# Performance work log

Hardware: AMD Instinct MI355X
Metric: run time of the kernel (lower is better)

## Reference

```python
import jax, jax.numpy as jnp
import numpy as np

DIM_IN = 1024
DIM_OUT = 1024
N_HOST = 4096
N_GUEST = 8192


def setup_inputs() -> dict:
    key = jax.random.key(0)
    k1, k2, k3, k4, k5 = jax.random.split(key, 5)
    # kaiming_uniform_ default: bound = sqrt(6 / fan_in) with a=sqrt(5) -> gain=sqrt(2/(1+5)); here approximate with uniform init
    bound = float(np.sqrt(6.0 / DIM_IN) / np.sqrt(3.0))
    features_host = jax.random.normal(k1, (N_HOST, DIM_IN), dtype=jnp.float32)
    features_guests = jax.random.normal(k2, (N_GUEST, DIM_IN), dtype=jnp.float32)
    Q = jax.random.uniform(k3, (DIM_IN, DIM_OUT), dtype=jnp.float32, minval=-bound, maxval=bound)
    K = jax.random.uniform(k4, (DIM_IN, DIM_OUT), dtype=jnp.float32, minval=-bound, maxval=bound)
    V = jax.random.uniform(k5, (DIM_IN, DIM_OUT), dtype=jnp.float32, minval=-bound, maxval=bound)
    return {"features_host": features_host, "features_guests": features_guests, "Q": Q, "K": K, "V": V}


def reference(features_host, features_guests, Q, K, V):
    # query: [N, d_out], key/value: [M, d_out]
    query = features_host @ Q
    key = features_guests @ K
    value = features_guests @ V
    scale = 1.0 / jnp.sqrt(jnp.asarray(DIM_OUT, dtype=query.dtype))
    att = jnp.einsum("nd,md->nm", query, key) * scale  # [N, M]
    attention = jax.nn.softmax(att, axis=1)
    # dropout(p=0.2) is identity in eval mode (deterministic reference)
    return attention @ value  # [N, d_out]
```

## Files before the change

### kernel.cpp

```cpp
#include <hip/hip_runtime.h>
#include <stdint.h>

typedef float f32x4 __attribute__((ext_vector_type(4)));
typedef short bf16x8 __attribute__((ext_vector_type(8)));
typedef unsigned short u16;
typedef u16 u16x4 __attribute__((ext_vector_type(4)));

__device__ __forceinline__ u16 f2bf(float f) {
    union { float f; uint32_t u; } v; v.f = f;
    uint32_t r = v.u + 0x7FFFu + ((v.u >> 16) & 1u);
    return (u16)(r >> 16);
}
__device__ __forceinline__ float bf2f(u16 b) {
    union { uint32_t u; float f; } v; v.u = ((uint32_t)b) << 16;
    return v.f;
}

__device__ __forceinline__ void gload16(u16* lds, const u16* g) {
    __builtin_amdgcn_global_load_lds(
        (const __attribute__((address_space(1))) void*)(uintptr_t)g,
        (__attribute__((address_space(3))) void*)(uint32_t)(uintptr_t)lds,
        16, 0, 0);
}

__device__ __forceinline__ int xcd_map(int bid, int nwg) {
    return (bid & 7) * (nwg >> 3) + (bid >> 3);
}

#define BK 32

__global__ __launch_bounds__(256)
void proj_gemm(const u16* __restrict__ host_bf, const u16* __restrict__ guests_bf,
               const u16* __restrict__ Qt, const u16* __restrict__ Kt,
               const u16* __restrict__ Vt,
               u16* __restrict__ query_bf, u16* __restrict__ key_bf,
               u16* __restrict__ value_t)
{
    __shared__ u16 a_s[128 * BK];
    __shared__ u16 b_s[128 * BK];
    const int id = xcd_map(blockIdx.x, 1280);

    const u16 *A, *B; u16* Crm = nullptr; int bm, bn; int group;
    if (id < 256)      { group = 0; A = host_bf;   B = Qt; Crm = query_bf; bm = (id >> 3) * 128;         bn = (id & 7) * 128; }
    else if (id < 768) { group = 1; A = guests_bf; B = Kt; Crm = key_bf;   bm = ((id - 256) >> 3) * 128; bn = ((id - 256) & 7) * 128; }
    else               { group = 2; A = guests_bf; B = Vt; Crm = nullptr;  bm = ((id - 768) >> 3) * 128; bn = ((id - 768) & 7) * 128; }

    const int tid  = threadIdx.x;
    const int lane = tid & 63;
    const int wid  = tid >> 6;
    const int lr   = lane & 15;
    const int kg   = lane >> 4;
    const int wm   = (wid >> 1) * 64;
    const int wn   = (wid & 1) * 64;
    const int srow = tid >> 2;
    const int scol = (tid & 3) * 8;

    const u16* Ar0 = A + (size_t)(bm + srow) * 1024 + scol;
    const u16* Ar1 = A + (size_t)(bm + 64 + srow) * 1024 + scol;
    const u16* Br0 = B + (size_t)(bn + srow) * 1024 + scol;
    const u16* Br1 = B + (size_t)(bn + 64 + srow) * 1024 + scol;
    u16* a_d0 = a_s + wid * 512;
    u16* a_d1 = a_s + 2048 + wid * 512;
    u16* b_d0 = b_s + wid * 512;
    u16* b_d1 = b_s + 2048 + wid * 512;

    f32x4 acc[4][4];
#pragma unroll
    for (int i = 0; i < 4; ++i)
#pragma unroll
        for (int j = 0; j < 4; ++j)
            acc[i][j] = (f32x4){0.f, 0.f, 0.f, 0.f};

    for (int k0 = 0; k0 < 1024; k0 += BK) {
        __syncthreads();
        gload16(a_d0, Ar0 + k0);
        gload16(a_d1, Ar1 + k0);
        gload16(b_d0, Br0 + k0);
        gload16(b_d1, Br1 + k0);
        __syncthreads();

        bf16x8 af[4], bfr[4];
#pragma unroll
        for (int i = 0; i < 4; ++i)
            af[i] = *(const bf16x8*)&a_s[(wm + i * 16 + lr) * BK + kg * 8];
#pragma unroll
        for (int j = 0; j < 4; ++j)
            bfr[j] = *(const bf16x8*)&b_s[(wn + j * 16 + lr) * BK + kg * 8];
#pragma unroll
        for (int i = 0; i < 4; ++i)
#pragma unroll
            for (int j = 0; j < 4; ++j)
                acc[i][j] = __builtin_amdgcn_mfma_f32_16x16x32_bf16(af[i], bfr[j], acc[i][j], 0, 0, 0);
    }

    const int r0 = kg * 4;
    if (group == 2) {
#pragma unroll
        for (int i = 0; i < 4; ++i) {
#pragma unroll
            for (int j = 0; j < 4; ++j) {
                const int col = bn + wn + j * 16 + lr;
                const int row = bm + wm + i * 16 + r0;
                u16x4 w;
#pragma unroll
                for (int r = 0; r < 4; ++r) w[r] = f2bf(acc[i][j][r]);
                *(u16x4*)&value_t[(size_t)col * 8192 + row] = w;
            }
        }
    } else {
        const float scale = (group == 0) ? 0.03125f : 1.0f;
#pragma unroll
        for (int i = 0; i < 4; ++i) {
#pragma unroll
            for (int j = 0; j < 4; ++j) {
                const int col = bn + wn + j * 16 + lr;
#pragma unroll
                for (int r = 0; r < 4; ++r) {
                    const int row = bm + wm + i * 16 + r0 + r;
                    Crm[(size_t)row * 1024 + col] = f2bf(acc[i][j][r] * scale);
                }
            }
        }
    }
}

__global__ __launch_bounds__(256)
void qkt_gemm(const u16* __restrict__ A, const u16* __restrict__ Bt,
              u16* __restrict__ Cb)
{
    __shared__ u16 a_s[128 * BK];
    __shared__ u16 b_s[128 * BK];
    const int lin = blockIdx.x + (blockIdx.y << 6);
    const int swz = xcd_map(lin, 2048);
    const int bm = (swz >> 6) * 128;
    const int bn = (swz & 63) * 128;

    const int tid  = threadIdx.x;
    const int lane = tid & 63;
    const int wid  = tid >> 6;
    const int lr   = lane & 15;
    const int kg   = lane >> 4;
    const int wm   = (wid >> 1) * 64;
    const int wn   = (wid & 1) * 64;
    const int srow = tid >> 2;
    const int scol = (tid & 3) * 8;

    const u16* Ar0 = A  + (size_t)(bm + srow) * 1024 + scol;
    const u16* Ar1 = A  + (size_t)(bm + 64 + srow) * 1024 + scol;
    const u16* Br0 = Bt + (size_t)(bn + srow) * 1024 + scol;
    const u16* Br1 = Bt + (size_t)(bn + 64 + srow) * 1024 + scol;
    u16* a_d0 = a_s + wid * 512;
    u16* a_d1 = a_s + 2048 + wid * 512;
    u16* b_d0 = b_s + wid * 512;
    u16* b_d1 = b_s + 2048 + wid * 512;

    f32x4 acc[4][4];
#pragma unroll
    for (int i = 0; i < 4; ++i)
#pragma unroll
        for (int j = 0; j < 4; ++j)
            acc[i][j] = (f32x4){0.f, 0.f, 0.f, 0.f};

    for (int k0 = 0; k0 < 1024; k0 += BK) {
        __syncthreads();
        gload16(a_d0, Ar0 + k0);
        gload16(a_d1, Ar1 + k0);
        gload16(b_d0, Br0 + k0);
        gload16(b_d1, Br1 + k0);
        __syncthreads();

        bf16x8 af[4], bfr[4];
#pragma unroll
        for (int i = 0; i < 4; ++i)
            af[i] = *(const bf16x8*)&a_s[(wm + i * 16 + lr) * BK + kg * 8];
#pragma unroll
        for (int j = 0; j < 4; ++j)
            bfr[j] = *(const bf16x8*)&b_s[(wn + j * 16 + lr) * BK + kg * 8];
#pragma unroll
        for (int i = 0; i < 4; ++i)
#pragma unroll
            for (int j = 0; j < 4; ++j)
                acc[i][j] = __builtin_amdgcn_mfma_f32_16x16x32_bf16(af[i], bfr[j], acc[i][j], 0, 0, 0);
    }

    const int r0 = kg * 4;
#pragma unroll
    for (int i = 0; i < 4; ++i) {
#pragma unroll
        for (int j = 0; j < 4; ++j) {
            const int col = bn + wn + j * 16 + lr;
#pragma unroll
            for (int r = 0; r < 4; ++r) {
                const int row = bm + wm + i * 16 + r0 + r;
                Cb[(size_t)row * 8192 + col] = f2bf(acc[i][j][r]);
            }
        }
    }
}

__global__ __launch_bounds__(256)
void pv_gemm(const u16* __restrict__ A, const u16* __restrict__ Bt,
             float* __restrict__ C0, float* __restrict__ C1, float* __restrict__ C2)
{
    __shared__ u16 a_s[128 * BK];
    __shared__ u16 b_s[128 * BK];
    const int swz = xcd_map(blockIdx.x, 768);
    const int z   = swz >> 8;
    const int rem = swz & 255;
    const int bm  = (rem >> 3) * 128;
    const int bn  = (rem & 7) * 128;

    const int tid  = threadIdx.x;
    const int lane = tid & 63;
    const int wid  = tid >> 6;
    const int lr   = lane & 15;
    const int kg   = lane >> 4;
    const int wm   = (wid >> 1) * 64;
    const int wn   = (wid & 1) * 64;
    const int srow = tid >> 2;
    const int scol = (tid & 3) * 8;

    const int kBeg = z * 2752;
    const int kEnd = (z == 2) ? 8192 : kBeg + 2752;
    float* Cv = (z == 0) ? C0 : (z == 1) ? C1 : C2;

    const u16* Ar0 = A  + (size_t)(bm + srow) * 8192 + scol;
    const u16* Ar1 = A  + (size_t)(bm + 64 + srow) * 8192 + scol;
    const u16* Br0 = Bt + (size_t)(bn + srow) * 8192 + scol;
    const u16* Br1 = Bt + (size_t)(bn + 64 + srow) * 8192 + scol;
    u16* a_d0 = a_s + wid * 512;
    u16* a_d1 = a_s + 2048 + wid * 512;
    u16* b_d0 = b_s + wid * 512;
    u16* b_d1 = b_s + 2048 + wid * 512;

    f32x4 acc[4][4];
#pragma unroll
    for (int i = 0; i < 4; ++i)
#pragma unroll
        for (int j = 0; j < 4; ++j)
            acc[i][j] = (f32x4){0.f, 0.f, 0.f, 0.f};

    for (int k0 = kBeg; k0 < kEnd; k0 += BK) {
        __syncthreads();
        gload16(a_d0, Ar0 + k0);
        gload16(a_d1, Ar1 + k0);
        gload16(b_d0, Br0 + k0);
        gload16(b_d1, Br1 + k0);
        __syncthreads();

        bf16x8 af[4], bfr[4];
#pragma unroll
        for (int i = 0; i < 4; ++i)
            af[i] = *(const bf16x8*)&a_s[(wm + i * 16 + lr) * BK + kg * 8];
#pragma unroll
        for (int j = 0; j < 4; ++j)
            bfr[j] = *(const bf16x8*)&b_s[(wn + j * 16 + lr) * BK + kg * 8];
#pragma unroll
        for (int i = 0; i < 4; ++i)
#pragma unroll
            for (int j = 0; j < 4; ++j)
                acc[i][j] = __builtin_amdgcn_mfma_f32_16x16x32_bf16(af[i], bfr[j], acc[i][j], 0, 0, 0);
    }

    const int r0 = kg * 4;
#pragma unroll
    for (int i = 0; i < 4; ++i) {
#pragma unroll
        for (int j = 0; j < 4; ++j) {
            const int col = bn + wn + j * 16 + lr;
#pragma unroll
            for (int r = 0; r < 4; ++r) {
                const int row = bm + wm + i * 16 + r0 + r;
                Cv[(size_t)row * 1024 + col] = acc[i][j][r];
            }
        }
    }
}

__global__ __launch_bounds__(256)
void wtrans(const float* __restrict__ Qw, const float* __restrict__ Kw,
            const float* __restrict__ Vw, u16* __restrict__ Qt,
            u16* __restrict__ Kt, u16* __restrict__ Vt)
{
    __shared__ u16 tile[64][65];
    const float* in = (blockIdx.z == 0) ? Qw : (blockIdx.z == 1) ? Kw : Vw;
    u16* out        = (blockIdx.z == 0) ? Qt : (blockIdx.z == 1) ? Kt : Vt;
    const int r0 = blockIdx.y * 64;
    const int c0 = blockIdx.x * 64;
    const int tr = threadIdx.x >> 2;
    const int tq = threadIdx.x & 3;

    const float* p = in + (size_t)(r0 + tr) * 1024 + c0 + tq * 16;
#pragma unroll
    for (int i = 0; i < 16; i += 4) {
        float4 v = *(const float4*)(p + i);
        tile[tq * 16 + i + 0][tr] = f2bf(v.x);
        tile[tq * 16 + i + 1][tr] = f2bf(v.y);
        tile[tq * 16 + i + 2][tr] = f2bf(v.z);
        tile[tq * 16 + i + 3][tr] = f2bf(v.w);
    }
    __syncthreads();

    u16 tmp[16];
#pragma unroll
    for (int i = 0; i < 16; ++i) tmp[i] = tile[tr][tq * 16 + i];
    bf16x8 w0, w1;
#pragma unroll
    for (int j = 0; j < 8; ++j) { w0[j] = (short)tmp[j]; w1[j] = (short)tmp[8 + j]; }
    u16* o = out + (size_t)(c0 + tr) * 1024 + r0 + tq * 16;
    *(bf16x8*)o       = w0;
    *(bf16x8*)(o + 8) = w1;
}

__global__ __launch_bounds__(256)
void cvt_inputs(const float* __restrict__ host, const float* __restrict__ guests,
                u16* __restrict__ host_bf, u16* __restrict__ guests_bf)
{
    int b = blockIdx.x;
    const float* in; u16* out;
    if (b < 2048) { in = host; out = host_bf; }
    else          { in = guests; out = guests_bf; b -= 2048; }
    const size_t i = ((size_t)b * 256 + threadIdx.x) * 8;
    float4 v0 = *(const float4*)(in + i);
    float4 v1 = *(const float4*)(in + i + 4);
    bf16x8 w;
    w[0] = (short)f2bf(v0.x); w[1] = (short)f2bf(v0.y);
    w[2] = (short)f2bf(v0.z); w[3] = (short)f2bf(v0.w);
    w[4] = (short)f2bf(v1.x); w[5] = (short)f2bf(v1.y);
    w[6] = (short)f2bf(v1.z); w[7] = (short)f2bf(v1.w);
    *(bf16x8*)(out + i) = w;
}

__global__ __launch_bounds__(256)
void add2_f32(float* __restrict__ out, const float* __restrict__ p1,
              const float* __restrict__ p2)
{
    const size_t i = ((size_t)blockIdx.x * 256 + threadIdx.x) * 4;
    float4 a = *(const float4*)(out + i);
    float4 b = *(const float4*)(p1 + i);
    float4 c = *(const float4*)(p2 + i);
    a.x += b.x + c.x; a.y += b.y + c.y; a.z += b.z + c.z; a.w += b.w + c.w;
    *(float4*)(out + i) = a;
}

__global__ __launch_bounds__(256)
void softmax_inplace(u16* __restrict__ att)
{
    const int tid = threadIdx.x;
    u16* p = att + (size_t)blockIdx.x * 8192;

    float x[32];
#pragma unroll
    for (int c = 0; c < 4; ++c) {
        bf16x8 v = *(const bf16x8*)(p + c * 2048 + tid * 8);
#pragma unroll
        for (int j = 0; j < 8; ++j) x[c * 8 + j] = bf2f((u16)v[j]);
    }

    float mx = -1e30f;
#pragma unroll
    for (int i = 0; i < 32; ++i) mx = fmaxf(mx, x[i]);
#pragma unroll
    for (int o = 32; o >= 1; o >>= 1) mx = fmaxf(mx, __shfl_xor(mx, o));

    __shared__ float red[8];
    const int wid = tid >> 6, lane = tid & 63;
    if (lane == 0) red[wid] = mx;
    __syncthreads();
    mx = fmaxf(fmaxf(red[0], red[1]), fmaxf(red[2], red[3]));

    float s = 0.f;
#pragma unroll
    for (int i = 0; i < 32; ++i) { x[i] = __expf(x[i] - mx); s += x[i]; }
#pragma unroll
    for (int o = 32; o >= 1; o >>= 1) s += __shfl_xor(s, o);
    if (lane == 0) red[4 + wid] = s;
    __syncthreads();
    s = red[4] + red[5] + red[6] + red[7];
    const float inv = 1.0f / s;

#pragma unroll
    for (int c = 0; c < 4; ++c) {
        bf16x8 w;
#pragma unroll
        for (int j = 0; j < 8; ++j) w[j] = (short)f2bf(x[c * 8 + j] * inv);
        *(bf16x8*)(p + c * 2048 + tid * 8) = w;
    }
}

extern "C" void kernel_launch(void* const* d_in, const int* in_sizes, int n_in,
                              void* d_out, int out_size, void* d_ws, size_t ws_size,
                              hipStream_t stream)
{
    const float* host   = (const float*)d_in[0];
    const float* guests = (const float*)d_in[1];
    const float* Qw     = (const float*)d_in[2];
    const float* Kw     = (const float*)d_in[3];
    const float* Vw     = (const float*)d_in[4];
    float* out = (float*)d_out;

    char* ws = (char*)d_ws;
    u16* att       = (u16*)(ws);
    u16* host_bf   = (u16*)(ws);
    u16* guests_bf = (u16*)(ws + ( 8ull << 20));
    u16* Qt        = (u16*)(ws + (24ull << 20));
    u16* Kt        = (u16*)(ws + (26ull << 20));
    u16* Vt        = (u16*)(ws + (28ull << 20));
    u16* query_bf  = (u16*)(ws + (64ull << 20));
    u16* key_bf    = (u16*)(ws + (72ull << 20));
    u16* value_t   = (u16*)(ws + (88ull << 20));
    float* part1   = (float*)(ws + (64ull << 20));
    float* part2   = (float*)(ws + (104ull << 20));

    dim3 blk(256);

    cvt_inputs<<<dim3(6144), blk, 0, stream>>>(host, guests, host_bf, guests_bf);
    wtrans<<<dim3(16, 16, 3), blk, 0, stream>>>(Qw, Kw, Vw, Qt, Kt, Vt);

    proj_gemm<<<dim3(1280), blk, 0, stream>>>(host_bf, guests_bf, Qt, Kt, Vt,
                                              query_bf, key_bf, value_t);

    qkt_gemm<<<dim3(64, 32), blk, 0, stream>>>(query_bf, key_bf, att);

    softmax_inplace<<<dim3(4096), blk, 0, stream>>>(att);

    pv_gemm<<<dim3(768), blk, 0, stream>>>(att, value_t, out, part1, part2);
    add2_f32<<<dim3(4096), blk, 0, stream>>>(out, part1, part2);
}
```

Baseline: 384.9 us.

## Replace QK^T and PV GEMMs with 256x256 double-buffered 8-wave pipelined kernel

Introduces a shared 256x256-tile GEMM core with 512 threads, BK=64, double-buffered LDS (128KB), an XOR-swizzled LDS layout, and interleaved global-to-LDS prefetch and MFMA phases using setprio and fine-grained barriers. The old 128x128 single-buffered kernels are replaced for both the score GEMM and the split-K PV GEMM. The aim is more data reuse per tile, hidden load latency and fewer LDS bank conflicts. In exchange, register pressure and LDS use per block go up. The PV grid shrinks to 192 blocks, which may underfill the CUs.

```diff
diff --git a/kernel.cpp b/kernel.cpp
--- a/kernel.cpp
+++ b/kernel.cpp
@@ -28,6 +28,205 @@
 }
 
 #define BK 32
+
+__device__ __forceinline__ void gemm256_core(
+    const u16* __restrict__ A, const u16* __restrict__ Bt,
+    int lda, int ldb, int bm, int bn, int kBeg, int nt,
+    u16* lds, f32x4 (&acc)[8][4])
+{
+    const int tid  = threadIdx.x;
+    const int lane = tid & 63;
+    const int wid  = tid >> 6;
+    const int lr   = lane & 15;
+    const int kg   = lane >> 4;
+    const int wr   = wid >> 2;
+    const int wc   = wid & 3;
+
+    const int sr = tid >> 3;
+    const int sc = ((tid & 7) ^ (sr & 7)) * 8;
+    const u16* As = A  + (size_t)(bm + sr) * lda + kBeg + sc;
+    const u16* Bs = Bt + (size_t)(bn + sr) * ldb + kBeg + sc;
+    const int ldsW = wid * 512;
+
+    int arow[8], brow[4], kc[2];
+#pragma unroll
+    for (int m = 0; m < 8; ++m) arow[m] = wr * 8192 + (m * 16 + lr) * 64;
+#pragma unroll
+    for (int n = 0; n < 4; ++n)
+        brow[n] = 16384 + (wc >> 1) * 8192 + ((wc & 1) * 64 + n * 16 + lr) * 64;
+#pragma unroll
+    for (int ks = 0; ks < 2; ++ks) kc[ks] = (ks * 32 + kg * 8) ^ ((lr & 7) * 8);
+
+#define STG_A(q, h, t) do { \
+        const u16* _s = As + (size_t)((h) * 128) * lda + (t) * 64; \
+        gload16(lds + (q) * 32768 + (h) * 8192 + ldsW, _s); \
+        gload16(lds + (q) * 32768 + (h) * 8192 + 4096 + ldsW, _s + (size_t)64 * lda); \
+    } while (0)
+#define STG_B(q, h, t) do { \
+        const u16* _s = Bs + (size_t)((h) * 128) * ldb + (t) * 64; \
+        gload16(lds + (q) * 32768 + 16384 + (h) * 8192 + ldsW, _s); \
+        gload16(lds + (q) * 32768 + 16384 + (h) * 8192 + 4096 + ldsW, _s + (size_t)64 * ldb); \
+    } while (0)
+
+    STG_A(0, 0, 0); STG_A(0, 1, 0); STG_B(0, 0, 0); STG_B(0, 1, 0);
+    STG_B(1, 0, 1); STG_B(1, 1, 1);
+    asm volatile("s_waitcnt vmcnt(4)" ::: "memory");
+    __builtin_amdgcn_s_barrier();
+
+    bf16x8 fa[4][2], fb[4][2];
+    for (int t = 0; t < nt; ++t) {
+        const int p  = t & 1;
+        const int pb = p * 32768;
+
+#pragma unroll
+        for (int m = 0; m < 4; ++m)
+#pragma unroll
+            for (int ks = 0; ks < 2; ++ks)
+                fa[m][ks] = *(const bf16x8*)&lds[pb + arow[m] + kc[ks]];
+#pragma unroll
+        for (int n = 0; n < 2; ++n)
+#pragma unroll
+            for (int ks = 0; ks < 2; ++ks)
+                fb[n][ks] = *(const bf16x8*)&lds[pb + brow[n] + kc[ks]];
+        if (t + 1 < nt) STG_A(p ^ 1, 0, t + 1);
+        __builtin_amdgcn_s_barrier();
+        asm volatile("s_waitcnt lgkmcnt(0)" ::: "memory");
+        __builtin_amdgcn_sched_barrier(0);
+        __builtin_amdgcn_s_setprio(1);
+#pragma unroll
+        for (int ks = 0; ks < 2; ++ks)
+#pragma unroll
+            for (int m = 0; m < 4; ++m)
+#pragma unroll
+                for (int n = 0; n < 2; ++n)
+                    acc[m][n] = __builtin_amdgcn_mfma_f32_16x16x32_bf16(fa[m][ks], fb[n][ks], acc[m][n], 0, 0, 0);
+        __builtin_amdgcn_s_setprio(0);
+        __builtin_amdgcn_s_barrier();
+
+#pragma unroll
+        for (int n = 2; n < 4; ++n)
+#pragma unroll
+            for (int ks = 0; ks < 2; ++ks)
+                fb[n][ks] = *(const bf16x8*)&lds[pb + brow[n] + kc[ks]];
+        if (t + 1 < nt) STG_A(p ^ 1, 1, t + 1);
+        __builtin_amdgcn_s_barrier();
+        asm volatile("s_waitcnt lgkmcnt(0)" ::: "memory");
+        __builtin_amdgcn_sched_barrier(0);
+        __builtin_amdgcn_s_setprio(1);
+#pragma unroll
+        for (int ks = 0; ks < 2; ++ks)
+#pragma unroll
+            for (int m = 0; m < 4; ++m)
+#pragma unroll
+                for (int n = 2; n < 4; ++n)
+                    acc[m][n] = __builtin_amdgcn_mfma_f32_16x16x32_bf16(fa[m][ks], fb[n][ks], acc[m][n], 0, 0, 0);
+        __builtin_amdgcn_s_setprio(0);
+        __builtin_amdgcn_s_barrier();
+
+#pragma unroll
+        for (int m = 0; m < 4; ++m)
+#pragma unroll
+            for (int ks = 0; ks < 2; ++ks)
+                fa[m][ks] = *(const bf16x8*)&lds[pb + arow[4 + m] + kc[ks]];
+        if (t + 2 < nt) STG_B(p, 0, t + 2);
+        __builtin_amdgcn_s_barrier();
+        asm volatile("s_waitcnt lgkmcnt(0)" ::: "memory");
+        __builtin_amdgcn_sched_barrier(0);
+        __builtin_amdgcn_s_setprio(1);
+#pragma unroll
+        for (int ks = 0; ks < 2; ++ks)
+#pragma unroll
+            for (int m = 0; m < 4; ++m)
+#pragma unroll
+                for (int n = 0; n < 2; ++n)
+                    acc[4 + m][n] = __builtin_amdgcn_mfma_f32_16x16x32_bf16(fa[m][ks], fb[n][ks], acc[4 + m][n], 0, 0, 0);
+        __builtin_amdgcn_s_setprio(0);
+        __builtin_amdgcn_s_barrier();
+
+        if (t + 2 < nt) STG_B(p, 1, t + 2);
+        __builtin_amdgcn_s_barrier();
+        __builtin_amdgcn_s_setprio(1);
+#pragma unroll
+        for (int ks = 0; ks < 2; ++ks)
+#pragma unroll
+            for (int m = 0; m < 4; ++m)
+#pragma unroll
+                for (int n = 2; n < 4; ++n)
+                    acc[4 + m][n] = __builtin_amdgcn_mfma_f32_16x16x32_bf16(fa[m][ks], fb[n][ks], acc[4 + m][n], 0, 0, 0);
+        __builtin_amdgcn_s_setprio(0);
+        if (t + 2 < nt)      asm volatile("s_waitcnt vmcnt(4)" ::: "memory");
+        else if (t + 1 < nt) asm volatile("s_waitcnt vmcnt(0)" ::: "memory");
+        __builtin_amdgcn_s_barrier();
+    }
+#undef STG_A
+#undef STG_B
+}
+
+__global__ __launch_bounds__(512, 2)
+void qkt256(const u16* __restrict__ A, const u16* __restrict__ Bt,
+            u16* __restrict__ C)
+{
+    __shared__ u16 lds[65536];
+    const int swz = xcd_map(blockIdx.x, 512);
+    const int bm = (swz >> 5) * 256;
+    const int bn = (swz & 31) * 256;
+    f32x4 acc[8][4];
+#pragma unroll
+    for (int m = 0; m < 8; ++m)
+#pragma unroll
+        for (int n = 0; n < 4; ++n) acc[m][n] = (f32x4){0.f, 0.f, 0.f, 0.f};
+    gemm256_core(A, Bt, 1024, 1024, bm, bn, 0, 16, lds, acc);
+
+    const int lane = threadIdx.x & 63, wid = threadIdx.x >> 6;
+    const int lr = lane & 15, kg = lane >> 4, wr = wid >> 2, wc = wid & 3;
+#pragma unroll
+    for (int m = 0; m < 8; ++m)
+#pragma unroll
+        for (int n = 0; n < 4; ++n) {
+            const int col = bn + wc * 64 + n * 16 + lr;
+#pragma unroll
+            for (int r = 0; r < 4; ++r) {
+                const int row = bm + wr * 128 + m * 16 + kg * 4 + r;
+                C[(size_t)row * 8192 + col] = f2bf(acc[m][n][r]);
+            }
+        }
+}
+
+__global__ __launch_bounds__(512, 2)
+void pv256(const u16* __restrict__ A, const u16* __restrict__ Bt,
+           float* __restrict__ C0, float* __restrict__ C1, float* __restrict__ C2)
+{
+    __shared__ u16 lds[65536];
+    const int swz = xcd_map(blockIdx.x, 192);
+    const int z   = swz >> 6;
+    const int rem = swz & 63;
+    const int bm  = (rem >> 2) * 256;
+    const int bn  = (rem & 3) * 256;
+    const int kBeg = z * 2752;
+    const int nt   = (z == 2) ? 42 : 43;
+    float* Cv = (z == 0) ? C0 : (z == 1) ? C1 : C2;
+
+    f32x4 acc[8][4];
+#pragma unroll
+    for (int m = 0; m < 8; ++m)
+#pragma unroll
+        for (int n = 0; n < 4; ++n) acc[m][n] = (f32x4){0.f, 0.f, 0.f, 0.f};
+    gemm256_core(A, Bt, 8192, 8192, bm, bn, kBeg, nt, lds, acc);
+
+    const int lane = threadIdx.x & 63, wid = threadIdx.x >> 6;
+    const int lr = lane & 15, kg = lane >> 4, wr = wid >> 2, wc = wid & 3;
+#pragma unroll
+    for (int m = 0; m < 8; ++m)
+#pragma unroll
+        for (int n = 0; n < 4; ++n) {
+            const int col = bn + wc * 64 + n * 16 + lr;
+#pragma unroll
+            for (int r = 0; r < 4; ++r) {
+                const int row = bm + wr * 128 + m * 16 + kg * 4 + r;
+                Cv[(size_t)row * 1024 + col] = acc[m][n][r];
+            }
+        }
+}
 
 __global__ __launch_bounds__(256)
 void proj_gemm(const u16* __restrict__ host_bf, const u16* __restrict__ guests_bf,
@@ -119,159 +318,6 @@
                     const int row = bm + wm + i * 16 + r0 + r;
                     Crm[(size_t)row * 1024 + col] = f2bf(acc[i][j][r] * scale);
                 }
-            }
-        }
-    }
-}
-
-__global__ __launch_bounds__(256)
-void qkt_gemm(const u16* __restrict__ A, const u16* __restrict__ Bt,
-              u16* __restrict__ Cb)
-{
-    __shared__ u16 a_s[128 * BK];
-    __shared__ u16 b_s[128 * BK];
-    const int lin = blockIdx.x + (blockIdx.y << 6);
-    const int swz = xcd_map(lin, 2048);
-    const int bm = (swz >> 6) * 128;
-    const int bn = (swz & 63) * 128;
-
-    const int tid  = threadIdx.x;
-    const int lane = tid & 63;
-    const int wid  = tid >> 6;
-    const int lr   = lane & 15;
-    const int kg   = lane >> 4;
-    const int wm   = (wid >> 1) * 64;
-    const int wn   = (wid & 1) * 64;
-    const int srow = tid >> 2;
-    const int scol = (tid & 3) * 8;
-
-    const u16* Ar0 = A  + (size_t)(bm + srow) * 1024 + scol;
-    const u16* Ar1 = A  + (size_t)(bm + 64 + srow) * 1024 + scol;
-    const u16* Br0 = Bt + (size_t)(bn + srow) * 1024 + scol;
-    const u16* Br1 = Bt + (size_t)(bn + 64 + srow) * 1024 + scol;
-    u16* a_d0 = a_s + wid * 512;
-    u16* a_d1 = a_s + 2048 + wid * 512;
-    u16* b_d0 = b_s + wid * 512;
-    u16* b_d1 = b_s + 2048 + wid * 512;
-
-    f32x4 acc[4][4];
-#pragma unroll
-    for (int i = 0; i < 4; ++i)
-#pragma unroll
-        for (int j = 0; j < 4; ++j)
-            acc[i][j] = (f32x4){0.f, 0.f, 0.f, 0.f};
-
-    for (int k0 = 0; k0 < 1024; k0 += BK) {
-        __syncthreads();
-        gload16(a_d0, Ar0 + k0);
-        gload16(a_d1, Ar1 + k0);
-        gload16(b_d0, Br0 + k0);
-        gload16(b_d1, Br1 + k0);
-        __syncthreads();
-
-        bf16x8 af[4], bfr[4];
-#pragma unroll
-        for (int i = 0; i < 4; ++i)
-            af[i] = *(const bf16x8*)&a_s[(wm + i * 16 + lr) * BK + kg * 8];
-#pragma unroll
-        for (int j = 0; j < 4; ++j)
-            bfr[j] = *(const bf16x8*)&b_s[(wn + j * 16 + lr) * BK + kg * 8];
-#pragma unroll
-        for (int i = 0; i < 4; ++i)
-#pragma unroll
-            for (int j = 0; j < 4; ++j)
-                acc[i][j] = __builtin_amdgcn_mfma_f32_16x16x32_bf16(af[i], bfr[j], acc[i][j], 0, 0, 0);
-    }
-
-    const int r0 = kg * 4;
-#pragma unroll
-    for (int i = 0; i < 4; ++i) {
-#pragma unroll
-        for (int j = 0; j < 4; ++j) {
-            const int col = bn + wn + j * 16 + lr;
-#pragma unroll
-            for (int r = 0; r < 4; ++r) {
-                const int row = bm + wm + i * 16 + r0 + r;
-                Cb[(size_t)row * 8192 + col] = f2bf(acc[i][j][r]);
-            }
-        }
-    }
-}
-
-__global__ __launch_bounds__(256)
-void pv_gemm(const u16* __restrict__ A, const u16* __restrict__ Bt,
-             float* __restrict__ C0, float* __restrict__ C1, float* __restrict__ C2)
-{
-    __shared__ u16 a_s[128 * BK];
-    __shared__ u16 b_s[128 * BK];
-    const int swz = xcd_map(blockIdx.x, 768);
-    const int z   = swz >> 8;
-    const int rem = swz & 255;
-    const int bm  = (rem >> 3) * 128;
-    const int bn  = (rem & 7) * 128;
-
-    const int tid  = threadIdx.x;
-    const int lane = tid & 63;
-    const int wid  = tid >> 6;
-    const int lr   = lane & 15;
-    const int kg   = lane >> 4;
-    const int wm   = (wid >> 1) * 64;
-    const int wn   = (wid & 1) * 64;
-    const int srow = tid >> 2;
-    const int scol = (tid & 3) * 8;
-
-    const int kBeg = z * 2752;
-    const int kEnd = (z == 2) ? 8192 : kBeg + 2752;
-    float* Cv = (z == 0) ? C0 : (z == 1) ? C1 : C2;
-
-    const u16* Ar0 = A  + (size_t)(bm + srow) * 8192 + scol;
-    const u16* Ar1 = A  + (size_t)(bm + 64 + srow) * 8192 + scol;
-    const u16* Br0 = Bt + (size_t)(bn + srow) * 8192 + scol;
-    const u16* Br1 = Bt + (size_t)(bn + 64 + srow) * 8192 + scol;
-    u16* a_d0 = a_s + wid * 512;
-    u16* a_d1 = a_s + 2048 + wid * 512;
-    u16* b_d0 = b_s + wid * 512;
-    u16* b_d1 = b_s + 2048 + wid * 512;
-
-    f32x4 acc[4][4];
-#pragma unroll
-    for (int i = 0; i < 4; ++i)
-#pragma unroll
-        for (int j = 0; j < 4; ++j)
-            acc[i][j] = (f32x4){0.f, 0.f, 0.f, 0.f};
-
-    for (int k0 = kBeg; k0 < kEnd; k0 += BK) {
-        __syncthreads();
-        gload16(a_d0, Ar0 + k0);
-        gload16(a_d1, Ar1 + k0);
-        gload16(b_d0, Br0 + k0);
-        gload16(b_d1, Br1 + k0);
-        __syncthreads();
-
-        bf16x8 af[4], bfr[4];
-#pragma unroll
-        for (int i = 0; i < 4; ++i)
-            af[i] = *(const bf16x8*)&a_s[(wm + i * 16 + lr) * BK + kg * 8];
-#pragma unroll
-        for (int j = 0; j < 4; ++j)
-            bfr[j] = *(const bf16x8*)&b_s[(wn + j * 16 + lr) * BK + kg * 8];
-#pragma unroll
-        for (int i = 0; i < 4; ++i)
-#pragma unroll
-            for (int j = 0; j < 4; ++j)
-                acc[i][j] = __builtin_amdgcn_mfma_f32_16x16x32_bf16(af[i], bfr[j], acc[i][j], 0, 0, 0);
-    }
-
-    const int r0 = kg * 4;
-#pragma unroll
-    for (int i = 0; i < 4; ++i) {
-#pragma unroll
-        for (int j = 0; j < 4; ++j) {
-            const int col = bn + wn + j * 16 + lr;
-#pragma unroll
-            for (int r = 0; r < 4; ++r) {
-                const int row = bm + wm + i * 16 + r0 + r;
-                Cv[(size_t)row * 1024 + col] = acc[i][j][r];
             }
         }
     }
@@ -420,10 +466,10 @@
     proj_gemm<<<dim3(1280), blk, 0, stream>>>(host_bf, guests_bf, Qt, Kt, Vt,
                                               query_bf, key_bf, value_t);
 
-    qkt_gemm<<<dim3(64, 32), blk, 0, stream>>>(query_bf, key_bf, att);
+    qkt256<<<dim3(512), dim3(512), 0, stream>>>(query_bf, key_bf, att);
 
     softmax_inplace<<<dim3(4096), blk, 0, stream>>>(att);
 
-    pv_gemm<<<dim3(768), blk, 0, stream>>>(att, value_t, out, part1, part2);
+    pv256<<<dim3(192), dim3(512), 0, stream>>>(att, value_t, out, part1, part2);
     add2_f32<<<dim3(4096), blk, 0, stream>>>(out, part1, part2);
 }
```

New measurement: 350.1 us. 1.1x faster.
